# Performance work log

Hardware: AMD Instinct MI355X
Metric: run time of the kernel (lower is better)

Reference implementation:

```python
import jax, jax.numpy as jnp
import numpy as np

N_NODES = 32767   # complete binary tree, depth 15
EMB_DIM = 256
HIDDEN = 256      # 'hidden_size' -> LSTM state is 2*HIDDEN
VOCAB = 32        # len(ExprNode.TYPE_LIST)


def setup_inputs() -> dict:
    key = jax.random.key(0)
    k1, k2, k3, k4, k5, k6 = jax.random.split(key, 6)
    H2 = 2 * HIDDEN
    types = jax.random.randint(k1, (N_NODES,), 0, VOCAB, dtype=jnp.int32)
    # complete binary tree: children of node i are 2i+1 / 2i+2; sentinel slot N = zero state
    idx = np.arange(N_NODES)
    a = 2 * idx + 1
    b = 2 * idx + 2
    a = np.where(a < N_NODES, a, N_NODES).astype(np.int32)
    b = np.where(b < N_NODES, b, N_NODES).astype(np.int32)
    scale = 1.0 / np.sqrt(H2)
    return {
        "types": types,
        "a_idx": jnp.asarray(a),
        "b_idx": jnp.asarray(b),
        "emb": jax.random.normal(k2, (VOCAB, EMB_DIM), jnp.float32) * 0.02,
        "W_ih": jax.random.normal(k3, (4 * H2, EMB_DIM), jnp.float32) * scale,
        "W_hh": jax.random.normal(k4, (4 * H2, H2), jnp.float32) * scale,
        "b_ih": jax.random.normal(k5, (4 * H2,), jnp.float32) * scale,
        "b_hh": jax.random.normal(k6, (4 * H2,), jnp.float32) * scale,
    }


def reference(types, a_idx, b_idx, emb, W_ih, W_hh, b_ih, b_hh):
    """Recursive binary tree-LSTM over topological (leaves-first) order.
    Each node's LSTM state has size 2H; a parent's incoming (h, c) is the concat
    of the first H entries of each child's state (zeros for missing children).
    Returns per-node hidden outputs [N, 2H] (the out_map, indexed by node id)."""
    N = types.shape[0]
    H2 = W_hh.shape[1]
    H = H2 // 2
    # batched input projection for all nodes at once: [N, 4*H2]
    x_proj = emb[types] @ W_ih.T + (b_ih + b_hh)
    Hs0 = jnp.zeros((N + 1, H2), x_proj.dtype)  # slot N = h0 (zeros)
    Cs0 = jnp.zeros((N + 1, H2), x_proj.dtype)
    order = jnp.arange(N - 1, -1, -1)  # children (higher index) before parents

    def step(carry, i):
        Hs, Cs = carry
        h = jnp.concatenate([Hs[a_idx[i], :H], Hs[b_idx[i], :H]])  # [2H]
        c = jnp.concatenate([Cs[a_idx[i], :H], Cs[b_idx[i], :H]])
        gates = x_proj[i] + W_hh @ h                 # [4*H2], torch gate order i,f,g,o
        ig, fg, gg, og = jnp.split(gates, 4)
        c_new = jax.nn.sigmoid(fg) * c + jax.nn.sigmoid(ig) * jnp.tanh(gg)
        h_new = jax.nn.sigmoid(og) * jnp.tanh(c_new)
        return (Hs.at[i].set(h_new), Cs.at[i].set(c_new)), h_new

    _, outs = jax.lax.scan(step, (Hs0, Cs0), order)
    return outs[::-1]  # reorder so row i is node i's output
```

## Files before the change

kernel.cpp:

```cpp
#include <hip/hip_runtime.h>
#include <hip/hip_bf16.h>


#define NNODES 32767

typedef __attribute__((ext_vector_type(8))) short bf16x8;
typedef __attribute__((ext_vector_type(4))) float f32x4;

typedef const __attribute__((address_space(1))) void* gptr_t;
typedef __attribute__((address_space(3))) void* lptr_t;

__device__ __forceinline__ float sigf(float x) { return 1.0f / (1.0f + __expf(-x)); }
__device__ __forceinline__ float tanhfast(float x) { return 2.0f / (1.0f + __expf(-2.0f * x)) - 1.0f; }

__device__ __forceinline__ short bf_hi(float x) {
    __hip_bfloat16 h = __float2bfloat16(x);
    return __builtin_bit_cast(short, h);
}
__device__ __forceinline__ float bf_f(short s) {
    __hip_bfloat16 h = __builtin_bit_cast(__hip_bfloat16, s);
    return __bfloat162float(h);
}
__device__ __forceinline__ void split8(const float* src, short* hi, short* lo) {
#pragma unroll
    for (int j = 0; j < 8; ++j) {
        float x = src[j];
        short h = bf_hi(x);
        hi[j] = h;
        lo[j] = bf_hi(x - bf_f(h));
    }
}

__global__ void proj_kernel(const float* __restrict__ emb, const float* __restrict__ W_ih,
                            const float* __restrict__ b_ih, const float* __restrict__ b_hh,
                            float* __restrict__ proj) {
    __shared__ float e[256];
    int v = blockIdx.x >> 3;
    int rc = blockIdx.x & 7;
    int t = threadIdx.x;
    e[t] = emb[v * 256 + t];
    __syncthreads();
    int r = rc * 256 + t;
    const float4* w4 = (const float4*)(W_ih + (size_t)r * 256);
    const float4* e4 = (const float4*)e;
    float acc = 0.f;
#pragma unroll 8
    for (int k = 0; k < 64; ++k) {
        float4 w = w4[k];
        float4 h = e4[k];
        acc += w.x * h.x + w.y * h.y + w.z * h.z + w.w * h.w;
    }
    proj[v * 2048 + r] = acc + b_ih[r] + b_hh[r];
}

__global__ void wpack_kernel(const float* __restrict__ W_hh,
                             short* __restrict__ Whi, short* __restrict__ Wlo) {
    int t = blockIdx.x * 256 + threadIdx.x;
    int lane = t & 63;
    int kt = (t >> 6) & 15;
    int ntile = t >> 10;
    int n = ntile * 16 + (lane & 15);
    int k0 = kt * 32 + (lane >> 4) * 8;
    const float* src = W_hh + (size_t)n * 512 + k0;
    short hi[8], lo[8];
    split8(src, hi, lo);
    *(bf16x8*)(Whi + (size_t)t * 8) = *(bf16x8*)hi;
    *(bf16x8*)(Wlo + (size_t)t * 8) = *(bf16x8*)lo;
}

__global__ void leaf_kernel(const int* __restrict__ types, const float* __restrict__ proj,
                            float* __restrict__ out, float* __restrict__ C256,
                            short* __restrict__ Hsplit) {
    int node = 16383 + blockIdx.x;
    int t = threadIdx.x;
    int tt = types[node];
    const float* p = proj + (size_t)tt * 2048;
    float gi = p[t];
    float gg = p[1024 + t];
    float go = p[1536 + t];
    float cn = sigf(gi) * tanhfast(gg);
    float hn = sigf(go) * tanhfast(cn);
    out[(size_t)node * 512 + t] = hn;
    C256[(size_t)node * 256 + t] = cn;
    short hi = bf_hi(hn);
    Hsplit[(size_t)node * 512 + t] = hi;
    Hsplit[(size_t)node * 512 + 256 + t] = bf_hi(hn - bf_f(hi));
    float gi2 = p[256 + t];
    float gg2 = p[1280 + t];
    float go2 = p[1792 + t];
    float cn2 = sigf(gi2) * tanhfast(gg2);
    float hn2 = sigf(go2) * tanhfast(cn2);
    out[(size_t)node * 512 + 256 + t] = hn2;
}

__global__ __launch_bounds__(256) void big_gemm_lstm_kernel(
    const int* __restrict__ a_idx, const int* __restrict__ b_idx,
    const int* __restrict__ types, float* __restrict__ out,
    const float* __restrict__ proj, float* __restrict__ C256,
    short* __restrict__ Hsplit, int node_base) {
    __shared__ __align__(16) short lds[2][16384];
    __shared__ int sA[128], sB[128], sT[128];

    const unsigned WOFF = 16777216u;

    int t = threadIdx.x;
    int lin = blockIdx.x;
    int xcd = lin & 7;
    int g = lin >> 3;
    int y = g & 15;
    int x = (g >> 4) * 8 + xcd;
    int node0 = node_base + x * 128;
    int j0 = y * 32;

    if (t < 128) {
        sA[t] = a_idx[node0 + t];
        sB[t] = b_idx[node0 + t];
        sT[t] = types[node0 + t];
    }
    __syncthreads();

    int w = t >> 6, lane = t & 63;
    int wm = w >> 1, wn = w & 1;

    unsigned b0[8], b1[8], sk;
    if (w < 2) {
        sk = 32u;
#pragma unroll
        for (int i = 0; i < 8; ++i) {
            int ca = w * 8 + i;
            int rl = lane >> 3;
            int r_loc = ca * 8 + rl;
            int j = (lane & 7) ^ rl;
            unsigned ks = (unsigned)(j >> 2) * 256u + (unsigned)(j & 3) * 8u;
            b0[i] = (unsigned)sA[r_loc] * 512u + ks;
            b1[i] = (unsigned)sB[r_loc] * 512u + ks;
        }
    } else {
        sk = 512u;
#pragma unroll
        for (int i = 0; i < 8; ++i) {
            int cc = (w - 2) * 8 + i;
            int nt = cc >> 1, part = cc & 1;
            int q = nt >> 1, sub = nt & 1;
            unsigned ntg = (unsigned)(q * 32 + y * 2 + sub);
            b0[i] = WOFF + ntg * 8192u + (unsigned)part * 1048576u + (unsigned)lane * 8u;
            b1[i] = b0[i] + 4096u;
        }
    }

    f32x4 acc[4][4];
#pragma unroll
    for (int i = 0; i < 4; ++i)
#pragma unroll
        for (int q = 0; q < 4; ++q) acc[i][q] = (f32x4){0.f, 0.f, 0.f, 0.f};

    auto stage = [&](int kt, int buf) {
#pragma unroll
        for (int i = 0; i < 8; ++i) {
            unsigned off = ((kt < 8) ? b0[i] : b1[i]) + (unsigned)(kt & 7) * sk;
            const short* gsrc = Hsplit + off;
            short* ldst = &lds[buf][(w * 8 + i) * 512];
            __builtin_amdgcn_global_load_lds((gptr_t)gsrc, (lptr_t)ldst, 16, 0, 0);
        }
    };

    auto compute = [&](int buf) {
        const short* L = lds[buf];
        int s = lane >> 4;
        bf16x8 ah[4], al[4];
#pragma unroll
        for (int i = 0; i < 4; ++i) {
            int m_loc = (wm * 4 + i) * 16 + (lane & 15);
            int ch = m_loc >> 3;
            int r = m_loc & 7;
            const short* base = L + ch * 512 + r * 64;
            ah[i] = *(const bf16x8*)&base[(s ^ r) * 8];
            al[i] = *(const bf16x8*)&base[((4 + s) ^ r) * 8];
        }
        __builtin_amdgcn_s_setprio(1);
#pragma unroll
        for (int q = 0; q < 4; ++q) {
            int nt = q * 2 + wn;
            bf16x8 bh = *(const bf16x8*)&L[(16 + nt * 2) * 512 + lane * 8];
            bf16x8 bl = *(const bf16x8*)&L[(17 + nt * 2) * 512 + lane * 8];
#pragma unroll
            for (int i = 0; i < 4; ++i) {
                acc[i][q] = __builtin_amdgcn_mfma_f32_16x16x32_bf16(ah[i], bh, acc[i][q], 0, 0, 0);
                acc[i][q] = __builtin_amdgcn_mfma_f32_16x16x32_bf16(ah[i], bl, acc[i][q], 0, 0, 0);
                acc[i][q] = __builtin_amdgcn_mfma_f32_16x16x32_bf16(al[i], bh, acc[i][q], 0, 0, 0);
            }
        }
        __builtin_amdgcn_s_setprio(0);
    };

    stage(0, 0);
    int cur = 0;
#pragma unroll 1
    for (int kt = 0; kt < 16; ++kt) {
        __builtin_amdgcn_s_barrier();
        if (kt < 15) stage(kt + 1, cur ^ 1);
        if (kt < 15) {
            asm volatile("s_waitcnt vmcnt(8)" ::: "memory");
        } else {
            asm volatile("s_waitcnt vmcnt(0)" ::: "memory");
        }
        __builtin_amdgcn_s_barrier();
        compute(cur);
        cur ^= 1;
    }

    int j = j0 + wn * 16 + (lane & 15);
    bool fh = (j < 256);
    int jc = j & 255;
#pragma unroll
    for (int i = 0; i < 4; ++i) {
        int mrow = wm * 64 + i * 16 + (lane >> 4) * 4;
#pragma unroll
        for (int r = 0; r < 4; ++r) {
            int m_loc = mrow + r;
            int node = node0 + m_loc;
            const float* p = proj + (size_t)sT[m_loc] * 2048 + j;
            float gi = acc[i][0][r] + p[0];
            float gf = acc[i][1][r] + p[512];
            float gg = acc[i][2][r] + p[1024];
            float go = acc[i][3][r] + p[1536];
            int child = fh ? sA[m_loc] : sB[m_loc];
            float c = C256[(size_t)child * 256 + jc];
            float cn = sigf(gf) * c + sigf(gi) * tanhfast(gg);
            float hn = sigf(go) * tanhfast(cn);
            out[(size_t)node * 512 + j] = hn;
            if (fh) {
                C256[(size_t)node * 256 + j] = cn;
                short hi = bf_hi(hn);
                Hsplit[(size_t)node * 512 + j] = hi;
                Hsplit[(size_t)node * 512 + 256 + j] = bf_hi(hn - bf_f(hi));
            }
        }
    }
}

__global__ __launch_bounds__(256) void gemm_lstm_kernel(
    const int* __restrict__ a_idx, const int* __restrict__ b_idx,
    const int* __restrict__ types, float* __restrict__ out,
    const short* __restrict__ Whi, const short* __restrict__ Wlo,
    const float* __restrict__ proj, float* __restrict__ C256,
    short* __restrict__ Hsplit, int node_base, int Jc) {
    __shared__ short Ahi[2][16][64][8];
    __shared__ short Alo[2][16][64][8];
    __shared__ int sA[32], sB[32], sT[32];
    int t = threadIdx.x;
    int node0 = node_base + blockIdx.x * 32;
    if (t < 32) {
        sA[t] = a_idx[node0 + t];
        sB[t] = b_idx[node0 + t];
        sT[t] = types[node0 + t];
    }
    __syncthreads();

#pragma unroll
    for (int it = 0; it < 8; ++it) {
        int c = it * 256 + t;
        int mt = c >> 10;
        int kt = (c >> 6) & 15;
        int lane = c & 63;
        int m_loc = mt * 16 + (lane & 15);
        int k0 = kt * 32 + (lane >> 4) * 8;
        int child = (k0 < 256) ? sA[m_loc] : sB[m_loc];
        const short* src = Hsplit + (size_t)child * 512 + (k0 & 255);
        *(bf16x8*)&Ahi[mt][kt][lane][0] = *(const bf16x8*)src;
        *(bf16x8*)&Alo[mt][kt][lane][0] = *(const bf16x8*)(src + 256);
    }
    __syncthreads();

    int w = t >> 6;
    int lane = t & 63;
    int jsteps = Jc >> 4;
    int jbase = blockIdx.y * Jc;

    auto epilogue = [&](int j0, f32x4 (&acc)[4][2]) {
        int j = j0 + (lane & 15);
        int jc = j & 255;
        bool fh = (j < 256);
#pragma unroll
        for (int mt = 0; mt < 2; ++mt) {
            int mrow = mt * 16 + (lane >> 4) * 4;
#pragma unroll
            for (int r = 0; r < 4; ++r) {
                int m_loc = mrow + r;
                int node = node0 + m_loc;
                const float* p = proj + (size_t)sT[m_loc] * 2048 + j;
                float gi = acc[0][mt][r] + p[0];
                float gf = acc[1][mt][r] + p[512];
                float gg = acc[2][mt][r] + p[1024];
                float go = acc[3][mt][r] + p[1536];
                int child = fh ? sA[m_loc] : sB[m_loc];
                float c = C256[(size_t)child * 256 + jc];
                float cn = sigf(gf) * c + sigf(gi) * tanhfast(gg);
                float hn = sigf(go) * tanhfast(cn);
                out[(size_t)node * 512 + j] = hn;
                if (fh) {
                    C256[(size_t)node * 256 + j] = cn;
                    short hi = bf_hi(hn);
                    Hsplit[(size_t)node * 512 + j] = hi;
                    Hsplit[(size_t)node * 512 + 256 + j] = bf_hi(hn - bf_f(hi));
                }
            }
        }
    };

    if (jsteps >= 4) {
        for (int js = w; js < jsteps; js += 4) {
            int j0 = jbase + js * 16;
            f32x4 acc[4][2];
#pragma unroll
            for (int q = 0; q < 4; ++q)
#pragma unroll
                for (int mt = 0; mt < 2; ++mt) acc[q][mt] = (f32x4){0.f, 0.f, 0.f, 0.f};
            int nt0 = j0 >> 4;
#pragma unroll 4
            for (int kt = 0; kt < 16; ++kt) {
                bf16x8 ah0 = *(const bf16x8*)&Ahi[0][kt][lane][0];
                bf16x8 al0 = *(const bf16x8*)&Alo[0][kt][lane][0];
                bf16x8 ah1 = *(const bf16x8*)&Ahi[1][kt][lane][0];
                bf16x8 al1 = *(const bf16x8*)&Alo[1][kt][lane][0];
#pragma unroll
                for (int q = 0; q < 4; ++q) {
                    int ntile = q * 32 + nt0;
                    size_t off = ((size_t)(ntile * 16 + kt) * 64 + lane) * 8;
                    bf16x8 bh = *(const bf16x8*)(Whi + off);
                    bf16x8 bl = *(const bf16x8*)(Wlo + off);
                    acc[q][0] = __builtin_amdgcn_mfma_f32_16x16x32_bf16(ah0, bh, acc[q][0], 0, 0, 0);
                    acc[q][0] = __builtin_amdgcn_mfma_f32_16x16x32_bf16(ah0, bl, acc[q][0], 0, 0, 0);
                    acc[q][0] = __builtin_amdgcn_mfma_f32_16x16x32_bf16(al0, bh, acc[q][0], 0, 0, 0);
                    acc[q][1] = __builtin_amdgcn_mfma_f32_16x16x32_bf16(ah1, bh, acc[q][1], 0, 0, 0);
                    acc[q][1] = __builtin_amdgcn_mfma_f32_16x16x32_bf16(ah1, bl, acc[q][1], 0, 0, 0);
                    acc[q][1] = __builtin_amdgcn_mfma_f32_16x16x32_bf16(al1, bh, acc[q][1], 0, 0, 0);
                }
            }
            epilogue(j0, acc);
        }
    } else {
        int js = w & 1;
        int khalf = w >> 1;
        int j0 = jbase + js * 16;
        f32x4 acc[4][2];
#pragma unroll
        for (int q = 0; q < 4; ++q)
#pragma unroll
            for (int mt = 0; mt < 2; ++mt) acc[q][mt] = (f32x4){0.f, 0.f, 0.f, 0.f};
        int nt0 = j0 >> 4;
        int kt0 = khalf * 8;
#pragma unroll 4
        for (int kt = kt0; kt < kt0 + 8; ++kt) {
            bf16x8 ah0 = *(const bf16x8*)&Ahi[0][kt][lane][0];
            bf16x8 al0 = *(const bf16x8*)&Alo[0][kt][lane][0];
            bf16x8 ah1 = *(const bf16x8*)&Ahi[1][kt][lane][0];
            bf16x8 al1 = *(const bf16x8*)&Alo[1][kt][lane][0];
#pragma unroll
            for (int q = 0; q < 4; ++q) {
                int ntile = q * 32 + nt0;
                size_t off = ((size_t)(ntile * 16 + kt) * 64 + lane) * 8;
                bf16x8 bh = *(const bf16x8*)(Whi + off);
                bf16x8 bl = *(const bf16x8*)(Wlo + off);
                acc[q][0] = __builtin_amdgcn_mfma_f32_16x16x32_bf16(ah0, bh, acc[q][0], 0, 0, 0);
                acc[q][0] = __builtin_amdgcn_mfma_f32_16x16x32_bf16(ah0, bl, acc[q][0], 0, 0, 0);
                acc[q][0] = __builtin_amdgcn_mfma_f32_16x16x32_bf16(al0, bh, acc[q][0], 0, 0, 0);
                acc[q][1] = __builtin_amdgcn_mfma_f32_16x16x32_bf16(ah1, bh, acc[q][1], 0, 0, 0);
                acc[q][1] = __builtin_amdgcn_mfma_f32_16x16x32_bf16(ah1, bl, acc[q][1], 0, 0, 0);
                acc[q][1] = __builtin_amdgcn_mfma_f32_16x16x32_bf16(al1, bh, acc[q][1], 0, 0, 0);
            }
        }
        __syncthreads();
        float* xch = (float*)&Ahi[0][0][0][0];
        if (khalf == 1) {
#pragma unroll
            for (int q = 0; q < 4; ++q)
#pragma unroll
                for (int mt = 0; mt < 2; ++mt)
                    *(f32x4*)&xch[(((q * 2 + mt) * 128) + js * 64 + lane) * 4] = acc[q][mt];
        }
        __syncthreads();
        if (khalf == 0) {
#pragma unroll
            for (int q = 0; q < 4; ++q)
#pragma unroll
                for (int mt = 0; mt < 2; ++mt) {
                    f32x4 o = *(const f32x4*)&xch[(((q * 2 + mt) * 128) + js * 64 + lane) * 4];
                    acc[q][mt] += o;
                }
            epilogue(j0, acc);
        }
    }
}

__global__ __launch_bounds__(256) void smallv2_gemm_kernel(
    const int* __restrict__ a_idx, const int* __restrict__ b_idx,
    const float* __restrict__ out, const short* __restrict__ Whi,
    float* __restrict__ part, int node_base, int B) {
    __shared__ float hs[16][64];
    const short* Wlo = Whi + 1048576;

    int t = threadIdx.x;
    int y = blockIdx.x, z = blockIdx.y;
    int r = y * 256 + t;
    int kbase = z * 64;

    if (t < B * 16) {
        int n = t >> 4;
        int f4 = t & 15;
        int node = node_base + n;
        int child = (kbase < 256) ? a_idx[node] : b_idx[node];
        float4 v = ((const float4*)(out + (size_t)child * 512 + (kbase & 255)))[f4];
        *(float4*)&hs[n][f4 * 4] = v;
    }
    __syncthreads();

    float wv[64];
#pragma unroll
    for (int u = 0; u < 8; ++u) {
        int k = kbase + u * 8;
        int kt = k >> 5;
        int sub = (k >> 3) & 3;
        size_t off = ((size_t)((r >> 4) * 16 + kt) * 64 + (sub << 4) + (r & 15)) * 8;
        bf16x8 hi = *(const bf16x8*)(Whi + off);
        bf16x8 lo = *(const bf16x8*)(Wlo + off);
#pragma unroll
        for (int e = 0; e < 8; ++e)
            wv[u * 8 + e] = bf_f(hi[e]) + bf_f(lo[e]);
    }

    for (int n = 0; n < B; ++n) {
        float acc = 0.f;
#pragma unroll
        for (int k = 0; k < 64; ++k) acc += wv[k] * hs[n][k];
        part[((size_t)z * B + n) * 2048 + r] = acc;
    }
}

__global__ void small_combine_kernel(
    const int* __restrict__ a_idx, const int* __restrict__ b_idx,
    const int* __restrict__ types, const float* __restrict__ part,
    const float* __restrict__ proj, float* __restrict__ C256,
    short* __restrict__ Hsplit, float* __restrict__ out, int node_base, int B) {
    int bi = blockIdx.x;
    int n = bi >> 1;
    int j = ((bi & 1) << 8) + threadIdx.x;
    int node = node_base + n;
    float g[4] = {0.f, 0.f, 0.f, 0.f};
    for (int z = 0; z < 8; ++z) {
        const float* p = part + ((size_t)z * B + n) * 2048;
#pragma unroll
        for (int q = 0; q < 4; ++q) g[q] += p[q * 512 + j];
    }
    const float* p = proj + (size_t)types[node] * 2048 + j;
    float gi = g[0] + p[0];
    float gf = g[1] + p[512];
    float gg = g[2] + p[1024];
    float go = g[3] + p[1536];
    int child = (j < 256) ? a_idx[node] : b_idx[node];
    float c = C256[(size_t)child * 256 + (j & 255)];
    float cn = sigf(gf) * c + sigf(gi) * tanhfast(gg);
    float hn = sigf(go) * tanhfast(cn);
    out[(size_t)node * 512 + j] = hn;
    if (j < 256) {
        C256[(size_t)node * 256 + j] = cn;
        short hi = bf_hi(hn);
        Hsplit[(size_t)node * 512 + j] = hi;
        Hsplit[(size_t)node * 512 + 256 + j] = bf_hi(hn - bf_f(hi));
    }
}

extern "C" void kernel_launch(void* const* d_in, const int* in_sizes, int n_in,
                              void* d_out, int out_size, void* d_ws, size_t ws_size,
                              hipStream_t stream) {
    const int* types = (const int*)d_in[0];
    const int* a_idx = (const int*)d_in[1];
    const int* b_idx = (const int*)d_in[2];
    const float* emb = (const float*)d_in[3];
    const float* W_ih = (const float*)d_in[4];
    const float* W_hh = (const float*)d_in[5];
    const float* b_ih = (const float*)d_in[6];
    const float* b_hh = (const float*)d_in[7];
    float* out = (float*)d_out;

    float* ws = (float*)d_ws;
    float* proj = ws;
    float* C256 = ws + 65536;
    short* Hsplit = (short*)(C256 + 8388352);
    short* Whi = Hsplit + 16777216;
    short* Wlo = Whi + 1048576;
    float* part = (float*)(Wlo + 1048576);

    proj_kernel<<<256, 256, 0, stream>>>(emb, W_ih, b_ih, b_hh, proj);
    wpack_kernel<<<512, 256, 0, stream>>>(W_hh, Whi, Wlo);
    leaf_kernel<<<16384, 256, 0, stream>>>(types, proj, out, C256, Hsplit);

    for (int d = 13; d >= 0; --d) {
        int base = (1 << d) - 1;
        int B = 1 << d;
        if (B >= 2048) {
            int X = B / 128;
            big_gemm_lstm_kernel<<<X * 16, 256, 0, stream>>>(
                a_idx, b_idx, types, out, proj, C256, Hsplit, base);
        } else if (B >= 32) {
            int bx = B / 32;
            int J = 2;
            while (bx * J < 512 && J < 16) J <<= 1;
            gemm_lstm_kernel<<<dim3(bx, J), 256, 0, stream>>>(
                a_idx, b_idx, types, out, Whi, Wlo, proj, C256, Hsplit, base, 512 / J);
        } else {
            smallv2_gemm_kernel<<<dim3(8, 8), 256, 0, stream>>>(
                a_idx, b_idx, out, Whi, part, base, B);
            small_combine_kernel<<<B * 2, 256, 0, stream>>>(
                a_idx, b_idx, types, part, proj, C256, Hsplit, out, base, B);
        }
    }
}
```

Before: 385.1 us.

## Fuse top tree levels into one persistent kernel with grid barriers

Replaces the per-level pairs of small GEMM and combine launches for the top five tree levels with one persistent 64-block kernel. It keeps the W_hh slice in registers across levels and separates phases with an atomic-based grid barrier. It also moves the B=2048 level from the big GEMM kernel to the mid-size kernel. This removes about ten kernel launches and the repeated weight reloads. In exchange it relies on all 64 blocks being co-resident and pays for spin-wait barriers.

```diff
diff --git a/kernel.cpp b/kernel.cpp
--- a/kernel.cpp
+++ b/kernel.cpp
@@ -31,9 +31,29 @@
     }
 }
 
+__device__ __forceinline__ void gbar(int* cnt, int* gen, int nb) {
+    __syncthreads();
+    __threadfence();
+    if (threadIdx.x == 0) {
+        int g = atomicAdd(gen, 0);
+        if (atomicAdd(cnt, 1) == nb - 1) {
+            atomicExch(cnt, 0);
+            atomicAdd(gen, 1);
+        } else {
+            while (atomicAdd(gen, 0) == g) { __builtin_amdgcn_s_sleep(8); }
+        }
+    }
+    __syncthreads();
+    __threadfence();
+}
+
 __global__ void proj_kernel(const float* __restrict__ emb, const float* __restrict__ W_ih,
                             const float* __restrict__ b_ih, const float* __restrict__ b_hh,
-                            float* __restrict__ proj) {
+                            float* __restrict__ proj, int* bar) {
+    if (blockIdx.x == 0 && threadIdx.x == 0) {
+        atomicExch(bar, 0);
+        atomicExch(bar + 1, 0);
+    }
     __shared__ float e[256];
     int v = blockIdx.x >> 3;
     int rc = blockIdx.x & 7;
@@ -393,27 +413,19 @@
     }
 }
 
-__global__ __launch_bounds__(256) void smallv2_gemm_kernel(
+__global__ __launch_bounds__(256) void tiny_fused_kernel(
     const int* __restrict__ a_idx, const int* __restrict__ b_idx,
-    const float* __restrict__ out, const short* __restrict__ Whi,
-    float* __restrict__ part, int node_base, int B) {
+    const int* __restrict__ types, const short* __restrict__ Whi,
+    const float* __restrict__ proj, float* __restrict__ C256,
+    float* __restrict__ out, float* __restrict__ part, int* bar) {
     __shared__ float hs[16][64];
     const short* Wlo = Whi + 1048576;
 
     int t = threadIdx.x;
-    int y = blockIdx.x, z = blockIdx.y;
+    int blk = blockIdx.x;
+    int y = blk >> 3, z = blk & 7;
     int r = y * 256 + t;
     int kbase = z * 64;
-
-    if (t < B * 16) {
-        int n = t >> 4;
-        int f4 = t & 15;
-        int node = node_base + n;
-        int child = (kbase < 256) ? a_idx[node] : b_idx[node];
-        float4 v = ((const float4*)(out + (size_t)child * 512 + (kbase & 255)))[f4];
-        *(float4*)&hs[n][f4 * 4] = v;
-    }
-    __syncthreads();
 
     float wv[64];
 #pragma unroll
@@ -429,44 +441,53 @@
             wv[u * 8 + e] = bf_f(hi[e]) + bf_f(lo[e]);
     }
 
-    for (int n = 0; n < B; ++n) {
-        float acc = 0.f;
-#pragma unroll
-        for (int k = 0; k < 64; ++k) acc += wv[k] * hs[n][k];
-        part[((size_t)z * B + n) * 2048 + r] = acc;
-    }
-}
-
-__global__ void small_combine_kernel(
-    const int* __restrict__ a_idx, const int* __restrict__ b_idx,
-    const int* __restrict__ types, const float* __restrict__ part,
-    const float* __restrict__ proj, float* __restrict__ C256,
-    short* __restrict__ Hsplit, float* __restrict__ out, int node_base, int B) {
-    int bi = blockIdx.x;
-    int n = bi >> 1;
-    int j = ((bi & 1) << 8) + threadIdx.x;
-    int node = node_base + n;
-    float g[4] = {0.f, 0.f, 0.f, 0.f};
-    for (int z = 0; z < 8; ++z) {
-        const float* p = part + ((size_t)z * B + n) * 2048;
-#pragma unroll
-        for (int q = 0; q < 4; ++q) g[q] += p[q * 512 + j];
-    }
-    const float* p = proj + (size_t)types[node] * 2048 + j;
-    float gi = g[0] + p[0];
-    float gf = g[1] + p[512];
-    float gg = g[2] + p[1024];
-    float go = g[3] + p[1536];
-    int child = (j < 256) ? a_idx[node] : b_idx[node];
-    float c = C256[(size_t)child * 256 + (j & 255)];
-    float cn = sigf(gf) * c + sigf(gi) * tanhfast(gg);
-    float hn = sigf(go) * tanhfast(cn);
-    out[(size_t)node * 512 + j] = hn;
-    if (j < 256) {
-        C256[(size_t)node * 256 + j] = cn;
-        short hi = bf_hi(hn);
-        Hsplit[(size_t)node * 512 + j] = hi;
-        Hsplit[(size_t)node * 512 + 256 + j] = bf_hi(hn - bf_f(hi));
+#pragma unroll 1
+    for (int d = 4; d >= 0; --d) {
+        int base = (1 << d) - 1;
+        int B = 1 << d;
+        if (t < B * 16) {
+            int n = t >> 4, f4 = t & 15;
+            int node = base + n;
+            int child = (kbase < 256) ? a_idx[node] : b_idx[node];
+            const float* src = out + (size_t)child * 512 + (kbase & 255) + f4 * 4;
+            hs[n][f4 * 4 + 0] = src[0];
+            hs[n][f4 * 4 + 1] = src[1];
+            hs[n][f4 * 4 + 2] = src[2];
+            hs[n][f4 * 4 + 3] = src[3];
+        }
+        __syncthreads();
+#pragma unroll 1
+        for (int n = 0; n < B; ++n) {
+            float acc = 0.f;
+#pragma unroll
+            for (int k = 0; k < 64; ++k) acc += wv[k] * hs[n][k];
+            part[((size_t)z * B + n) * 2048 + r] = acc;
+        }
+        gbar(bar, bar + 1, 64);
+        if (blk < 2 * B) {
+            int n = blk >> 1;
+            int j = ((blk & 1) << 8) + t;
+            int node = base + n;
+            float g[4] = {0.f, 0.f, 0.f, 0.f};
+#pragma unroll 1
+            for (int zz = 0; zz < 8; ++zz) {
+                const float* p = part + ((size_t)zz * B + n) * 2048;
+#pragma unroll
+                for (int q = 0; q < 4; ++q) g[q] += p[q * 512 + j];
+            }
+            const float* p = proj + (size_t)types[node] * 2048 + j;
+            float gi = g[0] + p[0];
+            float gf = g[1] + p[512];
+            float gg = g[2] + p[1024];
+            float go = g[3] + p[1536];
+            int child = (j < 256) ? a_idx[node] : b_idx[node];
+            float c = C256[(size_t)child * 256 + (j & 255)];
+            float cn = sigf(gf) * c + sigf(gi) * tanhfast(gg);
+            float hn = sigf(go) * tanhfast(cn);
+            out[(size_t)node * 512 + j] = hn;
+            if (j < 256) C256[(size_t)node * 256 + j] = cn;
+        }
+        gbar(bar, bar + 1, 64);
     }
 }
 
@@ -490,29 +511,27 @@
     short* Whi = Hsplit + 16777216;
     short* Wlo = Whi + 1048576;
     float* part = (float*)(Wlo + 1048576);
-
-    proj_kernel<<<256, 256, 0, stream>>>(emb, W_ih, b_ih, b_hh, proj);
+    int* bar = (int*)(part + 262144);
+
+    proj_kernel<<<256, 256, 0, stream>>>(emb, W_ih, b_ih, b_hh, proj, bar);
     wpack_kernel<<<512, 256, 0, stream>>>(W_hh, Whi, Wlo);
     leaf_kernel<<<16384, 256, 0, stream>>>(types, proj, out, C256, Hsplit);
 
-    for (int d = 13; d >= 0; --d) {
+    for (int d = 13; d >= 5; --d) {
         int base = (1 << d) - 1;
         int B = 1 << d;
-        if (B >= 2048) {
+        if (B >= 4096) {
             int X = B / 128;
             big_gemm_lstm_kernel<<<X * 16, 256, 0, stream>>>(
                 a_idx, b_idx, types, out, proj, C256, Hsplit, base);
-        } else if (B >= 32) {
+        } else {
             int bx = B / 32;
             int J = 2;
             while (bx * J < 512 && J < 16) J <<= 1;
             gemm_lstm_kernel<<<dim3(bx, J), 256, 0, stream>>>(
                 a_idx, b_idx, types, out, Whi, Wlo, proj, C256, Hsplit, base, 512 / J);
-        } else {
-            smallv2_gemm_kernel<<<dim3(8, 8), 256, 0, stream>>>(
-                a_idx, b_idx, out, Whi, part, base, B);
-            small_combine_kernel<<<B * 2, 256, 0, stream>>>(
-                a_idx, b_idx, types, part, proj, C256, Hsplit, out, base, B);
-        }
-    }
-}
+        }
+    }
+    tiny_fused_kernel<<<64, 256, 0, stream>>>(
+        a_idx, b_idx, types, Whi, proj, C256, out, part, bar);
+}
```

Result: slower. 480.7 us (+24.8%).
